# Kernel optimization log

Measured on AMD Instinct MI355X. Metric: run time of the kernel, lower is better.

The kernel has to match this reference:

```python
import jax, jax.numpy as jnp
import numpy as np


def gcn_conv(x, W, b, src, dst, num_nodes):
    # PyG GCNConv: h = D^{-1/2} (A + I) D^{-1/2} (x W) + b
    h = x @ W  # [N, H]
    ones = jnp.ones(src.shape[0], dtype=h.dtype)
    deg = jax.ops.segment_sum(ones, dst, num_segments=num_nodes) + 1.0  # +1 for self-loop
    d_inv_sqrt = jax.lax.rsqrt(deg)
    norm = d_inv_sqrt[src] * d_inv_sqrt[dst]  # [E]
    msg = h[src] * norm[:, None]  # [E, H] gather
    agg = jax.ops.segment_sum(msg, dst, num_segments=num_nodes)  # scatter-add
    agg = agg + h * (1.0 / deg)[:, None]  # self-loop term: deg_i^{-1/2} * deg_i^{-1/2}
    return agg + b


def setup_inputs() -> dict:
    key = jax.random.key(0)
    ks = jax.random.split(key, 10)
    N, E, F, H, C, G = 100000, 1000000, 64, 128, 2, 512
    x = jax.random.normal(ks[0], (N, F), dtype=jnp.float32)
    edge_index = jax.random.randint(ks[1], (2, E), 0, N, dtype=jnp.int64)
    batch = jnp.sort(jax.random.randint(ks[2], (N,), 0, G, dtype=jnp.int64))
    s1 = 1.0 / np.sqrt(F)
    s2 = 1.0 / np.sqrt(H)
    W1 = jax.random.normal(ks[3], (F, H), dtype=jnp.float32) * s1
    b1 = jnp.zeros((H,), dtype=jnp.float32)
    W2 = jax.random.normal(ks[4], (H, H), dtype=jnp.float32) * s2
    b2 = jnp.zeros((H,), dtype=jnp.float32)
    Wfc = jax.random.normal(ks[5], (H, C), dtype=jnp.float32) * s2
    bfc = jnp.zeros((C,), dtype=jnp.float32)
    return {"x": x, "edge_index": edge_index, "batch": batch, "num_graphs": G,
            "W1": W1, "b1": b1, "W2": W2, "b2": b2, "Wfc": Wfc, "bfc": bfc}


def reference(x, edge_index, batch, num_graphs, W1, b1, W2, b2, Wfc, bfc):
    # Dropout is inference-mode (identity), matching model.eval().
    N = x.shape[0]
    src, dst = edge_index[0], edge_index[1]
    h = gcn_conv(x, W1, b1, src, dst, N)
    h = jax.nn.relu(h)
    h = gcn_conv(h, W2, b2, src, dst, N)
    h = jax.nn.relu(h)
    # global mean pool over graphs
    summed = jax.ops.segment_sum(h, batch, num_segments=num_graphs)  # [G, H]
    counts = jax.ops.segment_sum(jnp.ones((N,), h.dtype), batch, num_segments=num_graphs)
    pooled = summed / jnp.maximum(counts, 1.0)[:, None]
    logits = pooled @ Wfc + bfc  # [G, C]
    return jax.nn.softmax(logits, axis=1)
```

## Files before the change

### kernel.cpp

```cpp
#include <hip/hip_runtime.h>
#include <hip/hip_bf16.h>

typedef __hip_bfloat16 bf16;
typedef __attribute__((ext_vector_type(8))) short short8;
typedef __attribute__((ext_vector_type(4))) float f32x4;
typedef __attribute__((ext_vector_type(2))) float f32x2;

#define FDIM 64
#define HDIM 128

#define ESTRIDE 4096
#define EC 8192
#define ECPT (EC / 256)

__device__ __forceinline__ float b2f(bf16 v) { return __bfloat162float(v); }
__device__ __forceinline__ float bits2f(unsigned int u) {
    return __uint_as_float(u << 16);
}
__device__ __forceinline__ unsigned short f2bits(float f) {
    bf16 b = __float2bfloat16(f);
    return *reinterpret_cast<unsigned short*>(&b);
}
__device__ __forceinline__ unsigned char f2fp8(float v) {
    int pk = __builtin_amdgcn_cvt_pk_fp8_f32(v, v, 0, false);
    return (unsigned char)(pk & 0xFF);
}

__global__ __launch_bounds__(256) void k_prep_flags(const unsigned short* __restrict__ w1u,
                                                    const int* __restrict__ edge,
                                                    const int* __restrict__ batch,
                                                    int* __restrict__ flags,
                                                    int* __restrict__ zbase, int zn4) {
    if (blockIdx.x == 0 && threadIdx.x < 192) {
        int wave = threadIdx.x >> 6, lane = threadIdx.x & 63;
        if (wave == 0) {
            int wild = 0;
#pragma unroll
            for (int r = 0; r < 2; r++) {
                int i = 2 * lane + 128 * r;
                int e = (w1u[i] >> 7) & 0xFF;
                wild += (e == 0 || e >= 137) ? 1 : 0;
            }
            for (int s = 32; s; s >>= 1) wild += __shfl_down(wild, s);
            if (lane == 0) flags[0] = (wild > 16) ? 1 : 0;
        } else if (wave == 1) {
            int z = 0;
#pragma unroll
            for (int r = 0; r < 2; r++) {
                int i = 2 * lane + 1 + 128 * r;
                z += (edge[i] == 0) ? 1 : 0;
            }
            for (int s = 32; s; s >>= 1) z += __shfl_down(z, s);
            if (lane == 0) flags[1] = (z > 64) ? 1 : 0;
        } else {
            int z = 0;
#pragma unroll
            for (int r = 0; r < 2; r++) {
                int i = 1025 + 2 * lane + 128 * r;
                z += (batch[i] == 0) ? 1 : 0;
            }
            for (int s = 32; s; s >>= 1) z += __shfl_down(z, s);
            if (lane == 0) flags[2] = (z > 64) ? 1 : 0;
        }
    }
    int4 zz = make_int4(0, 0, 0, 0);
    int stride = gridDim.x * 256;
    for (int t = blockIdx.x * 256 + threadIdx.x; t < zn4; t += stride)
        ((int4*)zbase)[t] = zz;
}

__device__ __forceinline__ int edge_word(const int* e, long long logical_idx, int is64) {
    return is64 ? e[2 * logical_idx] : e[logical_idx];
}

__global__ __launch_bounds__(256) void k_phase1(const int* __restrict__ edge,
                                                int* __restrict__ gcur,
                                                int* __restrict__ ebuf,
                                                int E,
                                                const void* __restrict__ W1, const void* __restrict__ b1,
                                                const void* __restrict__ W2, const void* __restrict__ b2,
                                                const void* __restrict__ Wfc, const void* __restrict__ bfc,
                                                bf16* __restrict__ W1t, bf16* __restrict__ W2t,
                                                bf16* __restrict__ b1c, bf16* __restrict__ b2c,
                                                bf16* __restrict__ Wfcc, bf16* __restrict__ bfcc,
                                                const void* __restrict__ x,
                                                unsigned char* __restrict__ X8,
                                                int totalX4, const int* __restrict__ flags,
                                                const int* __restrict__ batch,
                                                int* __restrict__ gstart,
                                                int N, int G,
                                                int NB1, int WB, int XB) {
    int blk = blockIdx.x;
    if (blk < NB1) {
        __shared__ int h[512];
        int tid = threadIdx.x;
        for (int b2 = tid; b2 < 512; b2 += 256) h[b2] = 0;
        __syncthreads();
        int is64 = flags[1];
        int e0 = blk * EC;
        int dcache[ECPT];
#pragma unroll
        for (int k = 0; k < ECPT; k++) {
            int i = e0 + (k << 8) + tid;
            int d = -1;
            if (i < E) d = edge_word(edge, (long long)E + i, is64);
            dcache[k] = d;
            if (d >= 0) atomicAdd(&h[(d >> 8) & 511], 1);
        }
        __syncthreads();
        for (int b2 = tid; b2 < 512; b2 += 256) {
            int c = h[b2];
            h[b2] = c ? atomicAdd(&gcur[b2], c) : 0;
        }
        __syncthreads();
#pragma unroll
        for (int k = 0; k < ECPT; k++) {
            int i = e0 + (k << 8) + tid;
            int d = dcache[k];
            if (d >= 0) {
                int s = edge_word(edge, i, is64);
                int bb = (d >> 8) & 511;
                int pos = atomicAdd(&h[bb], 1);
                if ((unsigned)pos < (unsigned)ESTRIDE)
                    ebuf[(bb << 12) + pos] = s | ((d & 255) << 24);
            }
        }
    } else if (blk < NB1 + WB) {
        int f0 = flags[0];
        int gid = (blk - NB1) * 256 + threadIdx.x;
        int stride = WB * 256;
#define CV(src, si) (f0 ? __float2bfloat16(((const float*)(src))[si]) : ((const bf16*)(src))[si])
        for (int i = gid; i < FDIM * HDIM; i += stride) {
            int n = i >> 6, k = i & 63;
            W1t[i] = CV(W1, k * HDIM + n);
        }
        for (int i = gid; i < HDIM * HDIM; i += stride) {
            int n = i >> 7, k = i & 127;
            W2t[i] = CV(W2, k * HDIM + n);
        }
        for (int i = gid; i < HDIM; i += stride) b1c[i] = CV(b1, i);
        for (int i = gid; i < HDIM; i += stride) b2c[i] = CV(b2, i);
        for (int i = gid; i < HDIM * 2; i += stride) Wfcc[i] = CV(Wfc, i);
        for (int i = gid; i < 2; i += stride) bfcc[i] = CV(bfc, i);
#undef CV
    } else if (blk < NB1 + WB + XB) {
        int t = (blk - NB1 - WB) * 256 + threadIdx.x;
        if (t >= totalX4) return;
        float4 v;
        if (flags[0]) {
            v = ((const float4*)x)[t];
        } else {
            uint2 p = ((const uint2*)x)[t];
            v.x = bits2f(p.x & 0xFFFFu); v.y = bits2f(p.x >> 16);
            v.z = bits2f(p.y & 0xFFFFu); v.w = bits2f(p.y >> 16);
        }
        unsigned int q0 = (unsigned int)__builtin_amdgcn_cvt_pk_fp8_f32(v.x, v.y, 0, false) & 0xFFFFu;
        unsigned int q1 = (unsigned int)__builtin_amdgcn_cvt_pk_fp8_f32(v.z, v.w, 0, false) & 0xFFFFu;
        ((unsigned int*)X8)[t] = (q1 << 16) | q0;
    } else {
        int i = (blk - NB1 - WB - XB) * 256 + threadIdx.x;
        if (i >= N) return;
        int is64 = flags[2];
        int bi = is64 ? batch[2 * i] : batch[i];
        if (i == 0) {
            for (int g = 0; g <= bi; g++) gstart[g] = 0;
        } else {
            int bp = is64 ? batch[2 * (i - 1)] : batch[i - 1];
            for (int g = bp + 1; g <= bi; g++) gstart[g] = i;
        }
        if (i == N - 1) {
            for (int g = bi + 1; g <= G; g++) gstart[g] = N;
        }
    }
}

__global__ __launch_bounds__(256) void k_csr(const int* __restrict__ ebuf,
                                             const int* __restrict__ gcur,
                                             int* __restrict__ rowptr,
                                             int* __restrict__ cnt,
                                             float* __restrict__ dinv,
                                             int* __restrict__ srclist,
                                             int N) {
    __shared__ int sred[256];
    __shared__ int sc[256];
    __shared__ int sa[256], sb[256];
    int b = blockIdx.x;
    int tid = threadIdx.x;
    int part = 0;
    for (int j = tid; j < b; j += 256) {
        int v = gcur[j];
        part += (v > ESTRIDE) ? ESTRIDE : v;
    }
    sred[tid] = part;
    __syncthreads();
    for (int s = 128; s > 0; s >>= 1) {
        if (tid < s) sred[tid] += sred[tid + s];
        __syncthreads();
    }
    int gbase = sred[0];
    int cnt_b = gcur[b];
    if (cnt_b > ESTRIDE) cnt_b = ESTRIDE;
    sc[tid] = 0;
    __syncthreads();
    const int* eb = ebuf + (b << 12);
    for (int j = tid; j < cnt_b; j += 256) {
        int p = eb[j];
        atomicAdd(&sc[(unsigned)p >> 24], 1);
    }
    __syncthreads();
    int cval = sc[tid];
    sa[tid] = cval;
    __syncthreads();
    int* cur = sa; int* nxt = sb;
    for (int off = 1; off < 256; off <<= 1) {
        int v = cur[tid];
        if (tid >= off) v += cur[tid - off];
        nxt[tid] = v;
        __syncthreads();
        int* t = cur; cur = nxt; nxt = t;
    }
    int excl = cur[tid] - cval;
    int node = (b << 8) + tid;
    if (node < N) {
        rowptr[node] = gbase + excl;
        cnt[node] = cval;
        dinv[node] = rsqrtf((float)cval + 1.0f);
    }
    __syncthreads();
    sc[tid] = excl;
    __syncthreads();
    for (int j = tid; j < cnt_b; j += 256) {
        int p = eb[j];
        int pos = atomicAdd(&sc[(unsigned)p >> 24], 1);
        srclist[gbase + pos] = p & 0xFFFFFF;
    }
}

#define ACCFP8(u2, e) do { \
    f32x2 f01 = __builtin_amdgcn_cvt_pk_f32_fp8((u2).x, false); \
    f32x2 f23 = __builtin_amdgcn_cvt_pk_f32_fp8((u2).x, true); \
    f32x2 f45 = __builtin_amdgcn_cvt_pk_f32_fp8((u2).y, false); \
    f32x2 f67 = __builtin_amdgcn_cvt_pk_f32_fp8((u2).y, true); \
    acc[0] += f01[0] * (e); acc[1] += f01[1] * (e); \
    acc[2] += f23[0] * (e); acc[3] += f23[1] * (e); \
    acc[4] += f45[0] * (e); acc[5] += f45[1] * (e); \
    acc[6] += f67[0] * (e); acc[7] += f67[1] * (e); } while (0)

__global__ __launch_bounds__(256) void k_agg64(const unsigned char* __restrict__ x8,
                                               const int* __restrict__ srclist,
                                               const int* __restrict__ rowptr,
                                               const int* __restrict__ count,
                                               const float* __restrict__ dinv,
                                               bf16* __restrict__ outb, int N) {
    int wave = threadIdx.x >> 6;
    int lane = threadIdx.x & 63;
    int group = lane >> 3;
    int sub = lane & 7;
    int i = blockIdx.x * 32 + wave * 8 + group;
    if (i >= N) return;
    int start = rowptr[i];
    int cnt = count[i];
    float di = dinv[i];
    const uint2* hrow = (const uint2*)x8;
    float acc[8] = {0.f, 0.f, 0.f, 0.f, 0.f, 0.f, 0.f, 0.f};
    int lb = group << 3;
    for (int jb = 0; jb < cnt; jb += 8) {
        int m = cnt - jb; if (m > 8) m = 8;
        int sv = srclist[start + jb + ((sub < m) ? sub : (m - 1))];
        float dvv = dinv[sv];
        int j = 0;
        for (; j + 4 <= m; j += 4) {
            int s0 = __shfl(sv, lb + j + 0); float e0 = __shfl(dvv, lb + j + 0);
            int s1 = __shfl(sv, lb + j + 1); float e1 = __shfl(dvv, lb + j + 1);
            int s2 = __shfl(sv, lb + j + 2); float e2 = __shfl(dvv, lb + j + 2);
            int s3 = __shfl(sv, lb + j + 3); float e3 = __shfl(dvv, lb + j + 3);
            uint2 v0 = hrow[(size_t)s0 * 8 + sub];
            uint2 v1 = hrow[(size_t)s1 * 8 + sub];
            uint2 v2 = hrow[(size_t)s2 * 8 + sub];
            uint2 v3 = hrow[(size_t)s3 * 8 + sub];
            ACCFP8(v0, e0); ACCFP8(v1, e1); ACCFP8(v2, e2); ACCFP8(v3, e3);
        }
        for (; j < m; j++) {
            int s0 = __shfl(sv, lb + j); float e0 = __shfl(dvv, lb + j);
            uint2 v0 = hrow[(size_t)s0 * 8 + sub];
            ACCFP8(v0, e0);
        }
    }
    {
        uint2 vs = hrow[(size_t)i * 8 + sub];
        float self = di * di;
        float sacc[8] = {0.f};
        {
            float* acc = sacc;
            ACCFP8(vs, self);
        }
#pragma unroll
        for (int k = 0; k < 8; k++) acc[k] = di * acc[k] + sacc[k];
    }
    uint4 pv;
    pv.x = ((unsigned int)f2bits(acc[1]) << 16) | f2bits(acc[0]);
    pv.y = ((unsigned int)f2bits(acc[3]) << 16) | f2bits(acc[2]);
    pv.z = ((unsigned int)f2bits(acc[5]) << 16) | f2bits(acc[4]);
    pv.w = ((unsigned int)f2bits(acc[7]) << 16) | f2bits(acc[6]);
    ((uint4*)outb)[(size_t)i * 8 + sub] = pv;
}

__global__ __launch_bounds__(256) void k_agg128(const unsigned char* __restrict__ h8,
                                                const int* __restrict__ srclist,
                                                const int* __restrict__ rowptr,
                                                const int* __restrict__ count,
                                                const float* __restrict__ dinv,
                                                bf16* __restrict__ outb, int N) {
    int wave = threadIdx.x >> 6;
    int lane = threadIdx.x & 63;
    int group = lane >> 4;
    int sub = lane & 15;
    int i = blockIdx.x * 16 + wave * 4 + group;
    if (i >= N) return;
    int start = rowptr[i];
    int cnt = count[i];
    float di = dinv[i];
    const uint2* hrow = (const uint2*)h8;
    float acc[8] = {0.f, 0.f, 0.f, 0.f, 0.f, 0.f, 0.f, 0.f};
    int lb = group << 4;
    for (int jb = 0; jb < cnt; jb += 16) {
        int m = cnt - jb; if (m > 16) m = 16;
        int sv = srclist[start + jb + ((sub < m) ? sub : (m - 1))];
        float dvv = dinv[sv];
        int j = 0;
        for (; j + 4 <= m; j += 4) {
            int s0 = __shfl(sv, lb + j + 0); float e0 = __shfl(dvv, lb + j + 0);
            int s1 = __shfl(sv, lb + j + 1); float e1 = __shfl(dvv, lb + j + 1);
            int s2 = __shfl(sv, lb + j + 2); float e2 = __shfl(dvv, lb + j + 2);
            int s3 = __shfl(sv, lb + j + 3); float e3 = __shfl(dvv, lb + j + 3);
            uint2 v0 = hrow[(size_t)s0 * 16 + sub];
            uint2 v1 = hrow[(size_t)s1 * 16 + sub];
            uint2 v2 = hrow[(size_t)s2 * 16 + sub];
            uint2 v3 = hrow[(size_t)s3 * 16 + sub];
            ACCFP8(v0, e0); ACCFP8(v1, e1); ACCFP8(v2, e2); ACCFP8(v3, e3);
        }
        for (; j < m; j++) {
            int s0 = __shfl(sv, lb + j); float e0 = __shfl(dvv, lb + j);
            uint2 v0 = hrow[(size_t)s0 * 16 + sub];
            ACCFP8(v0, e0);
        }
    }
    {
        uint2 vs = hrow[(size_t)i * 16 + sub];
        float self = di * di;
        float sacc[8] = {0.f};
        {
            float* acc = sacc;
            ACCFP8(vs, self);
        }
#pragma unroll
        for (int k = 0; k < 8; k++) acc[k] = di * acc[k] + sacc[k];
    }
    uint4 pv;
    pv.x = ((unsigned int)f2bits(acc[1]) << 16) | f2bits(acc[0]);
    pv.y = ((unsigned int)f2bits(acc[3]) << 16) | f2bits(acc[2]);
    pv.z = ((unsigned int)f2bits(acc[5]) << 16) | f2bits(acc[4]);
    pv.w = ((unsigned int)f2bits(acc[7]) << 16) | f2bits(acc[6]);
    ((uint4*)outb)[(size_t)i * 16 + sub] = pv;
}

#define K1PAD 72
__global__ __launch_bounds__(256) void k_gemmA(const bf16* __restrict__ Y,
                                               const bf16* __restrict__ W1t,
                                               const bf16* __restrict__ bias,
                                               unsigned char* __restrict__ h8, int N) {
    __shared__ bf16 As[64 * K1PAD];
    __shared__ bf16 Wt[HDIM * K1PAD];
    __shared__ float bsf[HDIM];
    int tid = threadIdx.x;
    int base = blockIdx.x * 64;
    {
        const uint4* wsrc = (const uint4*)W1t;
        for (int i = tid; i < HDIM * 8; i += 256) {
            int n = i >> 3, c = i & 7;
            *(uint4*)&Wt[n * K1PAD + c * 8] = wsrc[n * 8 + c];
        }
    }
    {
        const uint4* xb = (const uint4*)Y;
        for (int i = tid; i < 64 * 8; i += 256) {
            int r = i >> 3, c = i & 7;
            int gr = base + r; if (gr >= N) gr = N - 1;
            *(uint4*)&As[r * K1PAD + c * 8] = xb[(size_t)gr * 8 + c];
        }
    }
    if (tid < HDIM) bsf[tid] = b2f(bias[tid]);
    __syncthreads();
    int wid = tid >> 6, lane = tid & 63;
    int l15 = lane & 15, q = lane >> 4;
    int m0 = wid * 16;
    short8 af[2];
#pragma unroll
    for (int kc = 0; kc < 2; kc++)
        af[kc] = *(const short8*)&As[(m0 + l15) * K1PAD + kc * 32 + q * 8];
    f32x4 acc[8];
#pragma unroll
    for (int nt = 0; nt < 8; nt++) {
        acc[nt] = (f32x4){0.f, 0.f, 0.f, 0.f};
#pragma unroll
        for (int kc = 0; kc < 2; kc++) {
            short8 bf = *(const short8*)&Wt[(nt * 16 + l15) * K1PAD + kc * 32 + q * 8];
            acc[nt] = __builtin_amdgcn_mfma_f32_16x16x32_bf16(af[kc], bf, acc[nt], 0, 0, 0);
        }
    }
#pragma unroll
    for (int nt = 0; nt < 8; nt++) {
        int col = nt * 16 + l15;
        float bv = bsf[col];
#pragma unroll
        for (int r = 0; r < 4; r++) {
            int gr = base + m0 + q * 4 + r;
            if (gr < N) {
                float v = fmaxf(acc[nt][r] + bv, 0.f);
                h8[(size_t)gr * HDIM + col] = f2fp8(v);
            }
        }
    }
}

#define K2PAD 136
__global__ __launch_bounds__(256) void k_gemmB(const bf16* __restrict__ Z,
                                               const bf16* __restrict__ W2t,
                                               const bf16* __restrict__ bias,
                                               bf16* __restrict__ outp, int N) {
    __shared__ bf16 As[64 * K2PAD];
    __shared__ bf16 Wt[HDIM * K2PAD];
    __shared__ float bsf[HDIM];
    int tid = threadIdx.x;
    int base = blockIdx.x * 64;
    {
        const uint4* wsrc = (const uint4*)W2t;
        for (int i = tid; i < HDIM * 16; i += 256) {
            int n = i >> 4, c = i & 15;
            *(uint4*)&Wt[n * K2PAD + c * 8] = wsrc[n * 16 + c];
        }
    }
    const uint4* xb = (const uint4*)Z;
    for (int i = tid; i < 64 * 16; i += 256) {
        int r = i >> 4, c = i & 15;
        int gr = base + r; if (gr >= N) gr = N - 1;
        *(uint4*)&As[r * K2PAD + c * 8] = xb[(size_t)gr * 16 + c];
    }
    if (tid < HDIM) bsf[tid] = b2f(bias[tid]);
    __syncthreads();
    int wid = tid >> 6, lane = tid & 63;
    int l15 = lane & 15, q = lane >> 4;
    int m0 = wid * 16;
    short8 af[4];
#pragma unroll
    for (int kc = 0; kc < 4; kc++)
        af[kc] = *(const short8*)&As[(m0 + l15) * K2PAD + kc * 32 + q * 8];
    f32x4 acc[8];
#pragma unroll
    for (int nt = 0; nt < 8; nt++) {
        acc[nt] = (f32x4){0.f, 0.f, 0.f, 0.f};
#pragma unroll
        for (int kc = 0; kc < 4; kc++) {
            short8 bf = *(const short8*)&Wt[(nt * 16 + l15) * K2PAD + kc * 32 + q * 8];
            acc[nt] = __builtin_amdgcn_mfma_f32_16x16x32_bf16(af[kc], bf, acc[nt], 0, 0, 0);
        }
    }
#pragma unroll
    for (int nt = 0; nt < 8; nt++) {
        int col = nt * 16 + l15;
        float bv = bsf[col];
#pragma unroll
        for (int r = 0; r < 4; r++) {
            int gr = base + m0 + q * 4 + r;
            if (gr < N) outp[(size_t)gr * HDIM + col] = __float2bfloat16(fmaxf(acc[nt][r] + bv, 0.f));
        }
    }
}

__global__ __launch_bounds__(256) void k_pool_sum(const bf16* __restrict__ hact,
                                                  const int* __restrict__ gstart,
                                                  float* __restrict__ Gsum,
                                                  float* __restrict__ Gcnt) {
    __shared__ float lds[16][HDIM + 1];
    int g = blockIdx.x;
    int s = gstart[g], e = gstart[g + 1];
    int tid = threadIdx.x;
    int cslot = tid & 15;
    int rslot = tid >> 4;
    const uint4* hp = (const uint4*)hact;
    float a[8] = {0.f, 0.f, 0.f, 0.f, 0.f, 0.f, 0.f, 0.f};
    for (int r = s + rslot; r < e; r += 16) {
        uint4 v = hp[(size_t)r * 16 + cslot];
        a[0] += bits2f(v.x & 0xFFFFu); a[1] += bits2f(v.x >> 16);
        a[2] += bits2f(v.y & 0xFFFFu); a[3] += bits2f(v.y >> 16);
        a[4] += bits2f(v.z & 0xFFFFu); a[5] += bits2f(v.z >> 16);
        a[6] += bits2f(v.w & 0xFFFFu); a[7] += bits2f(v.w >> 16);
    }
#pragma unroll
    for (int k = 0; k < 8; k++) lds[rslot][cslot * 8 + k] = a[k];
    __syncthreads();
    if (tid < HDIM) {
        float sum = 0.f;
#pragma unroll
        for (int k = 0; k < 16; k++) sum += lds[k][tid];
        Gsum[g * HDIM + tid] = sum;
        if (tid == 0) Gcnt[g] = (float)(e - s);
    }
}

__global__ __launch_bounds__(256) void k_pool_fc(const float* __restrict__ Gsum,
                                                 const float* __restrict__ Gcnt,
                                                 const bf16* __restrict__ Wfc,
                                                 const bf16* __restrict__ bfc,
                                                 void* __restrict__ out, int G,
                                                 const int* __restrict__ flags) {
    int wave = threadIdx.x >> 6, lane = threadIdx.x & 63;
    int g = blockIdx.x * 4 + wave;
    if (g >= G) return;
    float inv = 1.0f / fmaxf(Gcnt[g], 1.0f);
    float m0 = Gsum[g * HDIM + 2 * lane] * inv;
    float m1 = Gsum[g * HDIM + 2 * lane + 1] * inv;
    float l0 = m0 * b2f(Wfc[(2 * lane) * 2 + 0]) + m1 * b2f(Wfc[(2 * lane + 1) * 2 + 0]);
    float l1 = m0 * b2f(Wfc[(2 * lane) * 2 + 1]) + m1 * b2f(Wfc[(2 * lane + 1) * 2 + 1]);
    for (int s = 32; s; s >>= 1) { l0 += __shfl_down(l0, s); l1 += __shfl_down(l1, s); }
    if (lane == 0) {
        float z0 = l0 + b2f(bfc[0]);
        float z1 = l1 + b2f(bfc[1]);
        float mx = fmaxf(z0, z1);
        float e0 = expf(z0 - mx), e1 = expf(z1 - mx);
        float s = e0 + e1;
        float p0 = e0 / s, p1 = e1 / s;
        if (flags[0]) {
            ((float*)out)[2 * g + 0] = p0;
            ((float*)out)[2 * g + 1] = p1;
        } else {
            ((bf16*)out)[2 * g + 0] = __float2bfloat16(p0);
            ((bf16*)out)[2 * g + 1] = __float2bfloat16(p1);
        }
    }
}

extern "C" void kernel_launch(void* const* d_in, const int* in_sizes, int n_in,
                              void* d_out, int out_size, void* d_ws, size_t ws_size,
                              hipStream_t stream) {
    const void* x    = d_in[0];
    const int*  edge = (const int*)d_in[1];
    const int*  batch= (const int*)d_in[2];
    const void* W1  = d_in[4];
    const void* b1  = d_in[5];
    const void* W2  = d_in[6];
    const void* b2  = d_in[7];
    const void* Wfc = d_in[8];
    const void* bfc = d_in[9];

    int N = in_sizes[0] / FDIM;
    int E = in_sizes[1] / 2;
    int G = out_size / 2;

    int*   flags  = (int*)d_ws;
    float* dinv   = (float*)((char*)d_ws + 64);
    int*   gcur   = (int*)(dinv + N);
    int*   gstart = gcur + 512;
    float* Gsum   = (float*)(gstart + 516);
    float* Gcnt   = Gsum + (size_t)G * HDIM;
    int*   rowptr = (int*)(Gcnt + G);
    int*   count  = rowptr + N;
    int*   srclist= count + N;
    int*   ebuf   = srclist + E;
    bf16*  Abuf   = (bf16*)(ebuf + 512 * ESTRIDE);
    bf16*  Bbuf   = Abuf + (size_t)N * HDIM;
    bf16*  b1c    = Bbuf + (size_t)N * HDIM;
    bf16*  b2c    = b1c + HDIM;
    bf16*  Wfcc   = b2c + HDIM;
    bf16*  bfcc   = Wfcc + 256;
    bf16*  W1t    = bfcc + 64;
    bf16*  W2t    = W1t + FDIM * HDIM;
    unsigned char* H8 = (unsigned char*)(W2t + HDIM * HDIM);
    unsigned char* X8 = H8 + (size_t)N * HDIM;

    bf16* Y = Abuf;
    bf16* Z = Abuf;

    int NB  = (N + 255) >> 8;
    int NB1 = (E + EC - 1) / EC;
    int WB = 32;
    int XB = (N * 16 + 255) / 256;
    int BB = (N + 255) / 256;
    int totalX4 = N * 16;
    int zn4 = 512 / 4;

    k_prep_flags<<<64, 256, 0, stream>>>((const unsigned short*)W1, edge, batch, flags,
                                         gcur, zn4);
    k_phase1<<<NB1 + WB + XB + BB, 256, 0, stream>>>(edge, gcur, ebuf, E,
                                                     W1, b1, W2, b2, Wfc, bfc,
                                                     W1t, W2t, b1c, b2c, Wfcc, bfcc,
                                                     x, X8, totalX4, flags,
                                                     batch, gstart, N, G,
                                                     NB1, WB, XB);
    k_csr<<<NB, 256, 0, stream>>>(ebuf, gcur, rowptr, count, dinv, srclist, N);

    k_agg64<<<(N + 31) / 32, 256, 0, stream>>>(X8, srclist, rowptr, count, dinv, Y, N);
    k_gemmA<<<(N + 63) / 64, 256, 0, stream>>>(Y, W1t, b1c, H8, N);

    k_agg128<<<(N + 15) / 16, 256, 0, stream>>>(H8, srclist, rowptr, count, dinv, Z, N);
    k_gemmB<<<(N + 63) / 64, 256, 0, stream>>>(Z, W2t, b2c, Bbuf, N);

    k_pool_sum<<<G, 256, 0, stream>>>(Bbuf, gstart, Gsum, Gcnt);
    k_pool_fc<<<(G + 3) / 4, 256, 0, stream>>>(Gsum, Gcnt, Wfcc, bfcc, d_out, G, flags);
}
```

Baseline: 223.6 us.

## Fuse sparse aggregation into GEMM kernels and merge pooling with FC

Each layer's neighbor aggregation is moved into the GEMM kernel. Aggregated rows are written straight to LDS, so the intermediate bf16 buffer never goes through global memory. The pool-sum and pool-FC kernels are merged into one, and the flag-prep grid is shrunk. This removes three kernel launches and an N×128 bf16 round trip per layer. In exchange, the gather phase now runs at the GEMM's block granularity and with its LDS footprint, which may lower occupancy and latency hiding for the irregular gathers.

```diff
diff --git a/kernel.cpp b/kernel.cpp
--- a/kernel.cpp
+++ b/kernel.cpp
@@ -246,129 +246,15 @@
     acc[4] += f45[0] * (e); acc[5] += f45[1] * (e); \
     acc[6] += f67[0] * (e); acc[7] += f67[1] * (e); } while (0)
 
-__global__ __launch_bounds__(256) void k_agg64(const unsigned char* __restrict__ x8,
-                                               const int* __restrict__ srclist,
-                                               const int* __restrict__ rowptr,
-                                               const int* __restrict__ count,
-                                               const float* __restrict__ dinv,
-                                               bf16* __restrict__ outb, int N) {
-    int wave = threadIdx.x >> 6;
-    int lane = threadIdx.x & 63;
-    int group = lane >> 3;
-    int sub = lane & 7;
-    int i = blockIdx.x * 32 + wave * 8 + group;
-    if (i >= N) return;
-    int start = rowptr[i];
-    int cnt = count[i];
-    float di = dinv[i];
-    const uint2* hrow = (const uint2*)x8;
-    float acc[8] = {0.f, 0.f, 0.f, 0.f, 0.f, 0.f, 0.f, 0.f};
-    int lb = group << 3;
-    for (int jb = 0; jb < cnt; jb += 8) {
-        int m = cnt - jb; if (m > 8) m = 8;
-        int sv = srclist[start + jb + ((sub < m) ? sub : (m - 1))];
-        float dvv = dinv[sv];
-        int j = 0;
-        for (; j + 4 <= m; j += 4) {
-            int s0 = __shfl(sv, lb + j + 0); float e0 = __shfl(dvv, lb + j + 0);
-            int s1 = __shfl(sv, lb + j + 1); float e1 = __shfl(dvv, lb + j + 1);
-            int s2 = __shfl(sv, lb + j + 2); float e2 = __shfl(dvv, lb + j + 2);
-            int s3 = __shfl(sv, lb + j + 3); float e3 = __shfl(dvv, lb + j + 3);
-            uint2 v0 = hrow[(size_t)s0 * 8 + sub];
-            uint2 v1 = hrow[(size_t)s1 * 8 + sub];
-            uint2 v2 = hrow[(size_t)s2 * 8 + sub];
-            uint2 v3 = hrow[(size_t)s3 * 8 + sub];
-            ACCFP8(v0, e0); ACCFP8(v1, e1); ACCFP8(v2, e2); ACCFP8(v3, e3);
-        }
-        for (; j < m; j++) {
-            int s0 = __shfl(sv, lb + j); float e0 = __shfl(dvv, lb + j);
-            uint2 v0 = hrow[(size_t)s0 * 8 + sub];
-            ACCFP8(v0, e0);
-        }
-    }
-    {
-        uint2 vs = hrow[(size_t)i * 8 + sub];
-        float self = di * di;
-        float sacc[8] = {0.f};
-        {
-            float* acc = sacc;
-            ACCFP8(vs, self);
-        }
-#pragma unroll
-        for (int k = 0; k < 8; k++) acc[k] = di * acc[k] + sacc[k];
-    }
-    uint4 pv;
-    pv.x = ((unsigned int)f2bits(acc[1]) << 16) | f2bits(acc[0]);
-    pv.y = ((unsigned int)f2bits(acc[3]) << 16) | f2bits(acc[2]);
-    pv.z = ((unsigned int)f2bits(acc[5]) << 16) | f2bits(acc[4]);
-    pv.w = ((unsigned int)f2bits(acc[7]) << 16) | f2bits(acc[6]);
-    ((uint4*)outb)[(size_t)i * 8 + sub] = pv;
-}
-
-__global__ __launch_bounds__(256) void k_agg128(const unsigned char* __restrict__ h8,
-                                                const int* __restrict__ srclist,
-                                                const int* __restrict__ rowptr,
-                                                const int* __restrict__ count,
-                                                const float* __restrict__ dinv,
-                                                bf16* __restrict__ outb, int N) {
-    int wave = threadIdx.x >> 6;
-    int lane = threadIdx.x & 63;
-    int group = lane >> 4;
-    int sub = lane & 15;
-    int i = blockIdx.x * 16 + wave * 4 + group;
-    if (i >= N) return;
-    int start = rowptr[i];
-    int cnt = count[i];
-    float di = dinv[i];
-    const uint2* hrow = (const uint2*)h8;
-    float acc[8] = {0.f, 0.f, 0.f, 0.f, 0.f, 0.f, 0.f, 0.f};
-    int lb = group << 4;
-    for (int jb = 0; jb < cnt; jb += 16) {
-        int m = cnt - jb; if (m > 16) m = 16;
-        int sv = srclist[start + jb + ((sub < m) ? sub : (m - 1))];
-        float dvv = dinv[sv];
-        int j = 0;
-        for (; j + 4 <= m; j += 4) {
-            int s0 = __shfl(sv, lb + j + 0); float e0 = __shfl(dvv, lb + j + 0);
-            int s1 = __shfl(sv, lb + j + 1); float e1 = __shfl(dvv, lb + j + 1);
-            int s2 = __shfl(sv, lb + j + 2); float e2 = __shfl(dvv, lb + j + 2);
-            int s3 = __shfl(sv, lb + j + 3); float e3 = __shfl(dvv, lb + j + 3);
-            uint2 v0 = hrow[(size_t)s0 * 16 + sub];
-            uint2 v1 = hrow[(size_t)s1 * 16 + sub];
-            uint2 v2 = hrow[(size_t)s2 * 16 + sub];
-            uint2 v3 = hrow[(size_t)s3 * 16 + sub];
-            ACCFP8(v0, e0); ACCFP8(v1, e1); ACCFP8(v2, e2); ACCFP8(v3, e3);
-        }
-        for (; j < m; j++) {
-            int s0 = __shfl(sv, lb + j); float e0 = __shfl(dvv, lb + j);
-            uint2 v0 = hrow[(size_t)s0 * 16 + sub];
-            ACCFP8(v0, e0);
-        }
-    }
-    {
-        uint2 vs = hrow[(size_t)i * 16 + sub];
-        float self = di * di;
-        float sacc[8] = {0.f};
-        {
-            float* acc = sacc;
-            ACCFP8(vs, self);
-        }
-#pragma unroll
-        for (int k = 0; k < 8; k++) acc[k] = di * acc[k] + sacc[k];
-    }
-    uint4 pv;
-    pv.x = ((unsigned int)f2bits(acc[1]) << 16) | f2bits(acc[0]);
-    pv.y = ((unsigned int)f2bits(acc[3]) << 16) | f2bits(acc[2]);
-    pv.z = ((unsigned int)f2bits(acc[5]) << 16) | f2bits(acc[4]);
-    pv.w = ((unsigned int)f2bits(acc[7]) << 16) | f2bits(acc[6]);
-    ((uint4*)outb)[(size_t)i * 16 + sub] = pv;
-}
-
 #define K1PAD 72
-__global__ __launch_bounds__(256) void k_gemmA(const bf16* __restrict__ Y,
-                                               const bf16* __restrict__ W1t,
-                                               const bf16* __restrict__ bias,
-                                               unsigned char* __restrict__ h8, int N) {
+__global__ __launch_bounds__(256) void k_agg_gemmA(const unsigned char* __restrict__ x8,
+                                                   const int* __restrict__ srclist,
+                                                   const int* __restrict__ rowptr,
+                                                   const int* __restrict__ count,
+                                                   const float* __restrict__ dinv,
+                                                   const bf16* __restrict__ W1t,
+                                                   const bf16* __restrict__ bias,
+                                                   unsigned char* __restrict__ h8, int N) {
     __shared__ bf16 As[64 * K1PAD];
     __shared__ bf16 Wt[HDIM * K1PAD];
     __shared__ float bsf[HDIM];
@@ -381,19 +267,61 @@
             *(uint4*)&Wt[n * K1PAD + c * 8] = wsrc[n * 8 + c];
         }
     }
-    {
-        const uint4* xb = (const uint4*)Y;
-        for (int i = tid; i < 64 * 8; i += 256) {
-            int r = i >> 3, c = i & 7;
-            int gr = base + r; if (gr >= N) gr = N - 1;
-            *(uint4*)&As[r * K1PAD + c * 8] = xb[(size_t)gr * 8 + c];
-        }
-    }
     if (tid < HDIM) bsf[tid] = b2f(bias[tid]);
-    __syncthreads();
-    int wid = tid >> 6, lane = tid & 63;
+    int wave = tid >> 6, lane = tid & 63;
+    int group = lane >> 3, sub = lane & 7, lb = group << 3;
+    const uint2* hrow = (const uint2*)x8;
+#pragma unroll
+    for (int pass = 0; pass < 2; pass++) {
+        int r = pass * 32 + wave * 8 + group;
+        int i = base + r;
+        float acc[8] = {0.f, 0.f, 0.f, 0.f, 0.f, 0.f, 0.f, 0.f};
+        if (i < N) {
+            int start = rowptr[i];
+            int cnt = count[i];
+            float di = dinv[i];
+            for (int jb = 0; jb < cnt; jb += 8) {
+                int m = cnt - jb; if (m > 8) m = 8;
+                int sv = srclist[start + jb + ((sub < m) ? sub : (m - 1))];
+                float dvv = dinv[sv];
+                int j = 0;
+                for (; j + 4 <= m; j += 4) {
+                    int s0 = __shfl(sv, lb + j + 0); float e0 = __shfl(dvv, lb + j + 0);
+                    int s1 = __shfl(sv, lb + j + 1); float e1 = __shfl(dvv, lb + j + 1);
+                    int s2 = __shfl(sv, lb + j + 2); float e2 = __shfl(dvv, lb + j + 2);
+                    int s3 = __shfl(sv, lb + j + 3); float e3 = __shfl(dvv, lb + j + 3);
+                    uint2 v0 = hrow[(size_t)s0 * 8 + sub];
+                    uint2 v1 = hrow[(size_t)s1 * 8 + sub];
+                    uint2 v2 = hrow[(size_t)s2 * 8 + sub];
+                    uint2 v3 = hrow[(size_t)s3 * 8 + sub];
+                    ACCFP8(v0, e0); ACCFP8(v1, e1); ACCFP8(v2, e2); ACCFP8(v3, e3);
+                }
+                for (; j < m; j++) {
+                    int s0 = __shfl(sv, lb + j); float e0 = __shfl(dvv, lb + j);
+                    uint2 v0 = hrow[(size_t)s0 * 8 + sub];
+                    ACCFP8(v0, e0);
+                }
+            }
+            uint2 vs = hrow[(size_t)i * 8 + sub];
+            float self = di * di;
+            float sacc[8] = {0.f};
+            {
+                float* acc = sacc;
+                ACCFP8(vs, self);
+            }
+#pragma unroll
+            for (int k = 0; k < 8; k++) acc[k] = di * acc[k] + sacc[k];
+        }
+        uint4 pv;
+        pv.x = ((unsigned int)f2bits(acc[1]) << 16) | f2bits(acc[0]);
+        pv.y = ((unsigned int)f2bits(acc[3]) << 16) | f2bits(acc[2]);
+        pv.z = ((unsigned int)f2bits(acc[5]) << 16) | f2bits(acc[4]);
+        pv.w = ((unsigned int)f2bits(acc[7]) << 16) | f2bits(acc[6]);
+        *(uint4*)&As[r * K1PAD + sub * 8] = pv;
+    }
+    __syncthreads();
     int l15 = lane & 15, q = lane >> 4;
-    int m0 = wid * 16;
+    int m0 = wave * 16;
     short8 af[2];
 #pragma unroll
     for (int kc = 0; kc < 2; kc++)
@@ -424,10 +352,14 @@
 }
 
 #define K2PAD 136
-__global__ __launch_bounds__(256) void k_gemmB(const bf16* __restrict__ Z,
-                                               const bf16* __restrict__ W2t,
-                                               const bf16* __restrict__ bias,
-                                               bf16* __restrict__ outp, int N) {
+__global__ __launch_bounds__(256) void k_agg_gemmB(const unsigned char* __restrict__ h8,
+                                                   const int* __restrict__ srclist,
+                                                   const int* __restrict__ rowptr,
+                                                   const int* __restrict__ count,
+                                                   const float* __restrict__ dinv,
+                                                   const bf16* __restrict__ W2t,
+                                                   const bf16* __restrict__ bias,
+                                                   bf16* __restrict__ outp, int N) {
     __shared__ bf16 As[64 * K2PAD];
     __shared__ bf16 Wt[HDIM * K2PAD];
     __shared__ float bsf[HDIM];
@@ -440,17 +372,61 @@
             *(uint4*)&Wt[n * K2PAD + c * 8] = wsrc[n * 16 + c];
         }
     }
-    const uint4* xb = (const uint4*)Z;
-    for (int i = tid; i < 64 * 16; i += 256) {
-        int r = i >> 4, c = i & 15;
-        int gr = base + r; if (gr >= N) gr = N - 1;
-        *(uint4*)&As[r * K2PAD + c * 8] = xb[(size_t)gr * 16 + c];
-    }
     if (tid < HDIM) bsf[tid] = b2f(bias[tid]);
-    __syncthreads();
-    int wid = tid >> 6, lane = tid & 63;
+    int wave = tid >> 6, lane = tid & 63;
+    int group = lane >> 4, sub = lane & 15, lb = group << 4;
+    const uint2* hrow = (const uint2*)h8;
+#pragma unroll
+    for (int pass = 0; pass < 4; pass++) {
+        int r = pass * 16 + wave * 4 + group;
+        int i = base + r;
+        float acc[8] = {0.f, 0.f, 0.f, 0.f, 0.f, 0.f, 0.f, 0.f};
+        if (i < N) {
+            int start = rowptr[i];
+            int cnt = count[i];
+            float di = dinv[i];
+            for (int jb = 0; jb < cnt; jb += 16) {
+                int m = cnt - jb; if (m > 16) m = 16;
+                int sv = srclist[start + jb + ((sub < m) ? sub : (m - 1))];
+                float dvv = dinv[sv];
+                int j = 0;
+                for (; j + 4 <= m; j += 4) {
+                    int s0 = __shfl(sv, lb + j + 0); float e0 = __shfl(dvv, lb + j + 0);
+                    int s1 = __shfl(sv, lb + j + 1); float e1 = __shfl(dvv, lb + j + 1);
+                    int s2 = __shfl(sv, lb + j + 2); float e2 = __shfl(dvv, lb + j + 2);
+                    int s3 = __shfl(sv, lb + j + 3); float e3 = __shfl(dvv, lb + j + 3);
+                    uint2 v0 = hrow[(size_t)s0 * 16 + sub];
+                    uint2 v1 = hrow[(size_t)s1 * 16 + sub];
+                    uint2 v2 = hrow[(size_t)s2 * 16 + sub];
+                    uint2 v3 = hrow[(size_t)s3 * 16 + sub];
+                    ACCFP8(v0, e0); ACCFP8(v1, e1); ACCFP8(v2, e2); ACCFP8(v3, e3);
+                }
+                for (; j < m; j++) {
+                    int s0 = __shfl(sv, lb + j); float e0 = __shfl(dvv, lb + j);
+                    uint2 v0 = hrow[(size_t)s0 * 16 + sub];
+                    ACCFP8(v0, e0);
+                }
+            }
+            uint2 vs = hrow[(size_t)i * 16 + sub];
+            float self = di * di;
+            float sacc[8] = {0.f};
+            {
+                float* acc = sacc;
+                ACCFP8(vs, self);
+            }
+#pragma unroll
+            for (int k = 0; k < 8; k++) acc[k] = di * acc[k] + sacc[k];
+        }
+        uint4 pv;
+        pv.x = ((unsigned int)f2bits(acc[1]) << 16) | f2bits(acc[0]);
+        pv.y = ((unsigned int)f2bits(acc[3]) << 16) | f2bits(acc[2]);
+        pv.z = ((unsigned int)f2bits(acc[5]) << 16) | f2bits(acc[4]);
+        pv.w = ((unsigned int)f2bits(acc[7]) << 16) | f2bits(acc[6]);
+        *(uint4*)&As[r * K2PAD + sub * 8] = pv;
+    }
+    __syncthreads();
     int l15 = lane & 15, q = lane >> 4;
-    int m0 = wid * 16;
+    int m0 = wave * 16;
     short8 af[4];
 #pragma unroll
     for (int kc = 0; kc < 4; kc++)
@@ -477,11 +453,14 @@
     }
 }
 
-__global__ __launch_bounds__(256) void k_pool_sum(const bf16* __restrict__ hact,
-                                                  const int* __restrict__ gstart,
-                                                  float* __restrict__ Gsum,
-                                                  float* __restrict__ Gcnt) {
+__global__ __launch_bounds__(256) void k_pool(const bf16* __restrict__ hact,
+                                              const int* __restrict__ gstart,
+                                              const bf16* __restrict__ Wfc,
+                                              const bf16* __restrict__ bfc,
+                                              void* __restrict__ out,
+                                              const int* __restrict__ flags) {
     __shared__ float lds[16][HDIM + 1];
+    __shared__ float colsum[HDIM];
     int g = blockIdx.x;
     int s = gstart[g], e = gstart[g + 1];
     int tid = threadIdx.x;
@@ -503,33 +482,24 @@
         float sum = 0.f;
 #pragma unroll
         for (int k = 0; k < 16; k++) sum += lds[k][tid];
-        Gsum[g * HDIM + tid] = sum;
-        if (tid == 0) Gcnt[g] = (float)(e - s);
-    }
-}
-
-__global__ __launch_bounds__(256) void k_pool_fc(const float* __restrict__ Gsum,
-                                                 const float* __restrict__ Gcnt,
-                                                 const bf16* __restrict__ Wfc,
-                                                 const bf16* __restrict__ bfc,
-                                                 void* __restrict__ out, int G,
-                                                 const int* __restrict__ flags) {
-    int wave = threadIdx.x >> 6, lane = threadIdx.x & 63;
-    int g = blockIdx.x * 4 + wave;
-    if (g >= G) return;
-    float inv = 1.0f / fmaxf(Gcnt[g], 1.0f);
-    float m0 = Gsum[g * HDIM + 2 * lane] * inv;
-    float m1 = Gsum[g * HDIM + 2 * lane + 1] * inv;
+        colsum[tid] = sum;
+    }
+    __syncthreads();
+    if (tid >= 64) return;
+    int lane = tid;
+    float inv = 1.0f / fmaxf((float)(e - s), 1.0f);
+    float m0 = colsum[2 * lane] * inv;
+    float m1 = colsum[2 * lane + 1] * inv;
     float l0 = m0 * b2f(Wfc[(2 * lane) * 2 + 0]) + m1 * b2f(Wfc[(2 * lane + 1) * 2 + 0]);
     float l1 = m0 * b2f(Wfc[(2 * lane) * 2 + 1]) + m1 * b2f(Wfc[(2 * lane + 1) * 2 + 1]);
-    for (int s = 32; s; s >>= 1) { l0 += __shfl_down(l0, s); l1 += __shfl_down(l1, s); }
+    for (int sft = 32; sft; sft >>= 1) { l0 += __shfl_down(l0, sft); l1 += __shfl_down(l1, sft); }
     if (lane == 0) {
         float z0 = l0 + b2f(bfc[0]);
         float z1 = l1 + b2f(bfc[1]);
         float mx = fmaxf(z0, z1);
         float e0 = expf(z0 - mx), e1 = expf(z1 - mx);
-        float s = e0 + e1;
-        float p0 = e0 / s, p1 = e1 / s;
+        float sm = e0 + e1;
+        float p0 = e0 / sm, p1 = e1 / sm;
         if (flags[0]) {
             ((float*)out)[2 * g + 0] = p0;
             ((float*)out)[2 * g + 1] = p1;
@@ -561,14 +531,11 @@
     float* dinv   = (float*)((char*)d_ws + 64);
     int*   gcur   = (int*)(dinv + N);
     int*   gstart = gcur + 512;
-    float* Gsum   = (float*)(gstart + 516);
-    float* Gcnt   = Gsum + (size_t)G * HDIM;
-    int*   rowptr = (int*)(Gcnt + G);
+    int*   rowptr = gstart + 516;
     int*   count  = rowptr + N;
     int*   srclist= count + N;
     int*   ebuf   = srclist + E;
-    bf16*  Abuf   = (bf16*)(ebuf + 512 * ESTRIDE);
-    bf16*  Bbuf   = Abuf + (size_t)N * HDIM;
+    bf16*  Bbuf   = (bf16*)(ebuf + 512 * ESTRIDE);
     bf16*  b1c    = Bbuf + (size_t)N * HDIM;
     bf16*  b2c    = b1c + HDIM;
     bf16*  Wfcc   = b2c + HDIM;
@@ -578,9 +545,6 @@
     unsigned char* H8 = (unsigned char*)(W2t + HDIM * HDIM);
     unsigned char* X8 = H8 + (size_t)N * HDIM;
 
-    bf16* Y = Abuf;
-    bf16* Z = Abuf;
-
     int NB  = (N + 255) >> 8;
     int NB1 = (E + EC - 1) / EC;
     int WB = 32;
@@ -589,8 +553,8 @@
     int totalX4 = N * 16;
     int zn4 = 512 / 4;
 
-    k_prep_flags<<<64, 256, 0, stream>>>((const unsigned short*)W1, edge, batch, flags,
-                                         gcur, zn4);
+    k_prep_flags<<<4, 256, 0, stream>>>((const unsigned short*)W1, edge, batch, flags,
+                                        gcur, zn4);
     k_phase1<<<NB1 + WB + XB + BB, 256, 0, stream>>>(edge, gcur, ebuf, E,
                                                      W1, b1, W2, b2, Wfc, bfc,
                                                      W1t, W2t, b1c, b2c, Wfcc, bfcc,
@@ -599,12 +563,10 @@
                                                      NB1, WB, XB);
     k_csr<<<NB, 256, 0, stream>>>(ebuf, gcur, rowptr, count, dinv, srclist, N);
 
-    k_agg64<<<(N + 31) / 32, 256, 0, stream>>>(X8, srclist, rowptr, count, dinv, Y, N);
-    k_gemmA<<<(N + 63) / 64, 256, 0, stream>>>(Y, W1t, b1c, H8, N);
-
-    k_agg128<<<(N + 15) / 16, 256, 0, stream>>>(H8, srclist, rowptr, count, dinv, Z, N);
-    k_gemmB<<<(N + 63) / 64, 256, 0, stream>>>(Z, W2t, b2c, Bbuf, N);
-
-    k_pool_sum<<<G, 256, 0, stream>>>(Bbuf, gstart, Gsum, Gcnt);
-    k_pool_fc<<<(G + 3) / 4, 256, 0, stream>>>(Gsum, Gcnt, Wfcc, bfcc, d_out, G, flags);
-}
+    k_agg_gemmA<<<(N + 63) / 64, 256, 0, stream>>>(X8, srclist, rowptr, count, dinv,
+                                                   W1t, b1c, H8, N);
+    k_agg_gemmB<<<(N + 63) / 64, 256, 0, stream>>>(H8, srclist, rowptr, count, dinv,
+                                                   W2t, b2c, Bbuf, N);
+
+    k_pool<<<G, 256, 0, stream>>>(Bbuf, gstart, Wfcc, bfcc, d_out, flags);
+}
```

Result: slower. 233.9 us (+4.6%).
